# Kernel tuning notes

Hardware: AMD Instinct MI355X
Metric: run time of the kernel (lower is better)

The kernel has to match this reference:

```python
import jax, jax.numpy as jnp
import numpy as np

H = 768          # hidden size
NH = 12          # num heads
HD = H // NH     # head dim = 64
I = 3072         # intermediate size
EPS = 1e-6


def setup_inputs() -> dict:
    key = jax.random.key(0)
    ks = jax.random.split(key, 16)
    s = 1.0 / np.sqrt(H)
    si = 1.0 / np.sqrt(I)
    return {
        "hidden_states": jax.random.normal(ks[0], (16, 1024, H), jnp.float32),
        # attention projections (torch Linear: weight [out, in])
        "wq": jax.random.normal(ks[1], (H, H), jnp.float32) * s,
        "bq": jnp.zeros((H,), jnp.float32),
        "wk": jax.random.normal(ks[2], (H, H), jnp.float32) * s,
        "bk": jnp.zeros((H,), jnp.float32),
        "wv": jax.random.normal(ks[3], (H, H), jnp.float32) * s,
        "bv": jnp.zeros((H,), jnp.float32),
        "wo": jax.random.normal(ks[4], (H, H), jnp.float32) * s,
        "bo": jnp.zeros((H,), jnp.float32),
        # layer norms
        "ln1_g": jnp.ones((H,), jnp.float32),
        "ln1_b": jnp.zeros((H,), jnp.float32),
        "ln2_g": jnp.ones((H,), jnp.float32),
        "ln2_b": jnp.zeros((H,), jnp.float32),
        # MLP
        "w1": jax.random.normal(ks[5], (I, H), jnp.float32) * s,
        "b1": jnp.zeros((I,), jnp.float32),
        "w2": jax.random.normal(ks[6], (H, I), jnp.float32) * si,
        "b2": jnp.zeros((H,), jnp.float32),
    }


def _layer_norm(x, g, b):
    mu = jnp.mean(x, axis=-1, keepdims=True)
    var = jnp.var(x, axis=-1, keepdims=True)
    return (x - mu) * jax.lax.rsqrt(var + EPS) * g + b


def _linear(x, w, b):
    return jnp.einsum('bsi,oi->bso', x, w) + b


def reference(hidden_states, wq, bq, wk, bk, wv, bv, wo, bo,
              ln1_g, ln1_b, ln2_g, ln2_b, w1, b1, w2, b2):
    B, S, _ = hidden_states.shape
    scale = HD ** -0.5

    # attention block
    residual = hidden_states
    x = _layer_norm(hidden_states, ln1_g, ln1_b)
    q = _linear(x, wq, bq).reshape(B, S, NH, HD).transpose(0, 2, 1, 3)
    k = _linear(x, wk, bk).reshape(B, S, NH, HD).transpose(0, 2, 1, 3)
    v = _linear(x, wv, bv).reshape(B, S, NH, HD).transpose(0, 2, 1, 3)
    scores = jnp.einsum('bhqd,bhkd->bhqk', q, k) * scale   # [B,NH,S,S]
    attn = jax.nn.softmax(scores, axis=-1)
    o = jnp.einsum('bhqk,bhkd->bhqd', attn, v)
    o = o.transpose(0, 2, 1, 3).reshape(B, S, H)
    x = residual + _linear(o, wo, bo)

    # MLP block
    residual = x
    y = _layer_norm(x, ln2_g, ln2_b)
    y = jax.nn.gelu(_linear(y, w1, b1), approximate=True)  # tanh approx
    y = _linear(y, w2, b2)
    return residual + y
```

## Files before the change

### kernel.cpp

```cpp
#include <hip/hip_runtime.h>
#include <hip/hip_bf16.h>


#define H_ 768
#define I_ 3072
#define NTOK 16384
#define SEQ 1024
#define NH_ 12

typedef __attribute__((ext_vector_type(8))) __bf16 bf16x8;
typedef __attribute__((ext_vector_type(4))) __bf16 bf16x4;
typedef __attribute__((ext_vector_type(4))) float  f32x4;

__device__ __forceinline__ void gll16(const void* g, void* l) {
  __builtin_amdgcn_global_load_lds(
      (const __attribute__((address_space(1))) unsigned int*)g,
      (__attribute__((address_space(3))) unsigned int*)l, 16, 0, 0);
}

__global__ __launch_bounds__(256) void f2b(const float* __restrict__ s,
                                           __bf16* __restrict__ d, int n) {
  int i = (blockIdx.x * 256 + threadIdx.x) * 4;
  if (i >= n) return;
  f32x4 v = *(const f32x4*)&s[i];
  bf16x4 o;
  #pragma unroll
  for (int j = 0; j < 4; ++j) o[j] = (__bf16)v[j];
  *(bf16x4*)&d[i] = o;
}

__global__ __launch_bounds__(256) void ln_fwd(const float* __restrict__ x,
                                              const float* __restrict__ gg,
                                              const float* __restrict__ bb,
                                              __bf16* __restrict__ y) {
  const int row  = blockIdx.x * 4 + (threadIdx.x >> 6);
  const int lane = threadIdx.x & 63;
  const float* xr = x + (size_t)row * H_;
  f32x4 v[3];
  float s = 0.f, ss = 0.f;
  #pragma unroll
  for (int i = 0; i < 3; ++i) {
    v[i] = *(const f32x4*)&xr[lane * 4 + i * 256];
    #pragma unroll
    for (int j = 0; j < 4; ++j) { s += v[i][j]; ss += v[i][j] * v[i][j]; }
  }
  #pragma unroll
  for (int d = 1; d < 64; d <<= 1) { s += __shfl_xor(s, d); ss += __shfl_xor(ss, d); }
  const float mu   = s * (1.0f / 768.0f);
  const float var  = ss * (1.0f / 768.0f) - mu * mu;
  const float rstd = rsqrtf(var + 1e-6f);
  #pragma unroll
  for (int i = 0; i < 3; ++i) {
    const int c0 = lane * 4 + i * 256;
    f32x4 g4 = *(const f32x4*)&gg[c0];
    f32x4 b4 = *(const f32x4*)&bb[c0];
    bf16x4 o;
    #pragma unroll
    for (int j = 0; j < 4; ++j) o[j] = (__bf16)((v[i][j] - mu) * rstd * g4[j] + b4[j]);
    *(bf16x4*)&y[(size_t)row * H_ + c0] = o;
  }
}

template <int EPI>
__global__ __launch_bounds__(256) void gemm_bt(const __bf16* __restrict__ A,
                                               const __bf16* __restrict__ B,
                                               const float* __restrict__ bias,
                                               const float* __restrict__ res,
                                               void* __restrict__ Cv, int N, int K) {
  __shared__ __bf16 sA[128 * 64];
  __shared__ __bf16 sB[128 * 64];
  const int tid = threadIdx.x, lane = tid & 63, w = tid >> 6;
  const int lg = lane >> 4, lm = lane & 15;
  const int wr = w >> 1, wc = w & 1;
  const int m0 = blockIdx.y * 128, n0 = blockIdx.x * 128;
  const int rsub = lane >> 3;
  const int gcol = (lane & 7) ^ rsub;

  const __bf16* abase = A + (size_t)(m0 + w * 32 + rsub) * K + gcol * 8;
  const __bf16* bbase = B + (size_t)(n0 + w * 32 + rsub) * K + gcol * 8;

  f32x4 acc[4][4] = {};

  const int nkt = K >> 6;
  for (int kt = 0; kt < nkt; ++kt) {
    __syncthreads();
    #pragma unroll
    for (int j = 0; j < 4; ++j) {
      gll16(abase + (size_t)j * 8 * K + kt * 64, (char*)sA + (w * 4 + j) * 1024);
      gll16(bbase + (size_t)j * 8 * K + kt * 64, (char*)sB + (w * 4 + j) * 1024);
    }
    __syncthreads();

    bf16x8 af[4][2], bfr[4][2];
    #pragma unroll
    for (int f = 0; f < 4; ++f) {
      #pragma unroll
      for (int ks = 0; ks < 2; ++ks) {
        const int ra = wr * 64 + f * 16 + lm;
        const int pa = (lg + ks * 4) ^ (ra & 7);
        af[f][ks] = *(const bf16x8*)&sA[ra * 64 + pa * 8];
        const int rb = wc * 64 + f * 16 + lm;
        const int pb = (lg + ks * 4) ^ (rb & 7);
        bfr[f][ks] = *(const bf16x8*)&sB[rb * 64 + pb * 8];
      }
    }
    #pragma unroll
    for (int ks = 0; ks < 2; ++ks)
      #pragma unroll
      for (int mf = 0; mf < 4; ++mf)
        #pragma unroll
        for (int nf = 0; nf < 4; ++nf)
          acc[mf][nf] = __builtin_amdgcn_mfma_f32_16x16x32_bf16(
              af[mf][ks], bfr[nf][ks], acc[mf][nf], 0, 0, 0);
  }

  #pragma unroll
  for (int nf = 0; nf < 4; ++nf) {
    const int col = n0 + wc * 64 + nf * 16 + lm;
    const float bi = bias[col];
    #pragma unroll
    for (int mf = 0; mf < 4; ++mf) {
      #pragma unroll
      for (int q = 0; q < 4; ++q) {
        const size_t row = (size_t)(m0 + wr * 64 + mf * 16 + lg * 4 + q);
        float v = acc[mf][nf][q] + bi;
        if constexpr (EPI == 1) {
          const float u = 0.7978845608028654f * (v + 0.044715f * v * v * v);
          v = v / (1.0f + __expf(-2.0f * u));
        }
        if constexpr (EPI == 2) {
          v += res[row * N + col];
          ((float*)Cv)[row * N + col] = v;
        } else {
          ((__bf16*)Cv)[row * N + col] = (__bf16)v;
        }
      }
    }
  }
}

__global__ __launch_bounds__(256) void vtrans(const __bf16* __restrict__ qkv,
                                              __bf16* __restrict__ vt) {
  __shared__ __bf16 t[64][72];
  const int b = blockIdx.z, h = blockIdx.y, st = blockIdx.x;
  const int tid = threadIdx.x;
  const int r = tid >> 2, s2 = (tid & 3) * 2;
  const __bf16* src = qkv + (size_t)(b * SEQ + st * 64 + r) * 2304 + 1536 + h * 64;
  *(bf16x8*)&t[r][s2 * 8]     = *(const bf16x8*)&src[s2 * 8];
  *(bf16x8*)&t[r][s2 * 8 + 8] = *(const bf16x8*)&src[s2 * 8 + 8];
  __syncthreads();
  __bf16* dst = vt + (size_t)((b * NH_ + h) * 64 + r) * SEQ + st * 64;
  bf16x8 a, c;
  #pragma unroll
  for (int j = 0; j < 8; ++j) { a[j] = t[s2 * 8 + j][r]; c[j] = t[s2 * 8 + 8 + j][r]; }
  *(bf16x8*)&dst[s2 * 8]     = a;
  *(bf16x8*)&dst[s2 * 8 + 8] = c;
}

__global__ __launch_bounds__(256) void attn_fwd(const __bf16* __restrict__ qkv,
                                                const __bf16* __restrict__ vt,
                                                __bf16* __restrict__ o) {
  __shared__ __bf16 sK[64 * 64];
  __shared__ __bf16 sV[64 * 64];
  __shared__ __bf16 sP[4][32 * 64];
  const int b = blockIdx.z, h = blockIdx.y, qt = blockIdx.x;
  const int tid = threadIdx.x, lane = tid & 63, w = tid >> 6;
  const int lg = lane >> 4, lm = lane & 15;
  const size_t rowbase = (size_t)b * SEQ + qt * 128 + w * 32;

  bf16x8 qf[2][2];
  #pragma unroll
  for (int mf = 0; mf < 2; ++mf)
    #pragma unroll
    for (int ks = 0; ks < 2; ++ks) {
      const __bf16* src = qkv + (rowbase + mf * 16 + lm) * 2304 + h * 64 + lg * 8 + ks * 32;
      bf16x8 t = *(const bf16x8*)src;
      #pragma unroll
      for (int j = 0; j < 8; ++j) t[j] = (__bf16)((float)t[j] * 0.125f);
      qf[mf][ks] = t;
    }

  float mreg[2][4], lreg[2][4];
  f32x4 oacc[2][4] = {};
  #pragma unroll
  for (int mf = 0; mf < 2; ++mf)
    #pragma unroll
    for (int q = 0; q < 4; ++q) { mreg[mf][q] = -3.0e38f; lreg[mf][q] = 0.f; }

  const int rsub = lane >> 3;
  const int gcol = (lane & 7) ^ rsub;
  const __bf16* kbase = qkv + (size_t)b * SEQ * 2304 + 768 + h * 64 + gcol * 8;
  const __bf16* vbase = vt + (size_t)((b * NH_ + h) * 64) * SEQ + gcol * 8;

  for (int kt = 0; kt < 16; ++kt) {
    __syncthreads();
    #pragma unroll
    for (int i = 0; i < 2; ++i) {
      const int r = (w * 2 + i) * 8 + rsub;
      gll16(kbase + (size_t)(kt * 64 + r) * 2304, (char*)sK + (w * 2 + i) * 1024);
      gll16(vbase + (size_t)r * SEQ + kt * 64,    (char*)sV + (w * 2 + i) * 1024);
    }
    __syncthreads();

    f32x4 sc[2][4] = {};
    bf16x8 kf[4][2];
    #pragma unroll
    for (int nf = 0; nf < 4; ++nf)
      #pragma unroll
      for (int ks = 0; ks < 2; ++ks) {
        const int row = nf * 16 + lm;
        const int ph  = (lg + ks * 4) ^ (row & 7);
        kf[nf][ks] = *(const bf16x8*)&sK[row * 64 + ph * 8];
      }
    #pragma unroll
    for (int ks = 0; ks < 2; ++ks)
      #pragma unroll
      for (int mf = 0; mf < 2; ++mf)
        #pragma unroll
        for (int nf = 0; nf < 4; ++nf)
          sc[mf][nf] = __builtin_amdgcn_mfma_f32_16x16x32_bf16(
              qf[mf][ks], kf[nf][ks], sc[mf][nf], 0, 0, 0);

    #pragma unroll
    for (int mf = 0; mf < 2; ++mf) {
      #pragma unroll
      for (int q = 0; q < 4; ++q) {
        float tm = fmaxf(fmaxf(sc[mf][0][q], sc[mf][1][q]),
                         fmaxf(sc[mf][2][q], sc[mf][3][q]));
        tm = fmaxf(tm, __shfl_xor(tm, 1));
        tm = fmaxf(tm, __shfl_xor(tm, 2));
        tm = fmaxf(tm, __shfl_xor(tm, 4));
        tm = fmaxf(tm, __shfl_xor(tm, 8));
        const float mo = mreg[mf][q];
        const float mn = fmaxf(mo, tm);
        const float f  = __expf(mo - mn);
        mreg[mf][q] = mn;
        float rs = 0.f;
        #pragma unroll
        for (int nf = 0; nf < 4; ++nf) {
          const float p = __expf(sc[mf][nf][q] - mn);
          sc[mf][nf][q] = p;
          rs += p;
        }
        rs += __shfl_xor(rs, 1); rs += __shfl_xor(rs, 2);
        rs += __shfl_xor(rs, 4); rs += __shfl_xor(rs, 8);
        lreg[mf][q] = lreg[mf][q] * f + rs;
        #pragma unroll
        for (int nd = 0; nd < 4; ++nd) oacc[mf][nd][q] *= f;
      }
    }

    __bf16* pw = sP[w];
    #pragma unroll
    for (int mf = 0; mf < 2; ++mf)
      #pragma unroll
      for (int nf = 0; nf < 4; ++nf)
        #pragma unroll
        for (int q = 0; q < 4; ++q) {
          const int row = mf * 16 + lg * 4 + q;
          const int col = nf * 16 + lm;
          const int ph  = (col >> 3) ^ (row & 7);
          pw[row * 64 + ph * 8 + (col & 7)] = (__bf16)sc[mf][nf][q];
        }
    asm volatile("s_waitcnt lgkmcnt(0)" ::: "memory");

    bf16x8 pf[2][2], vf[4][2];
    #pragma unroll
    for (int mf = 0; mf < 2; ++mf)
      #pragma unroll
      for (int ks = 0; ks < 2; ++ks) {
        const int row = mf * 16 + lm;
        const int ph  = (lg + ks * 4) ^ (row & 7);
        pf[mf][ks] = *(const bf16x8*)&pw[row * 64 + ph * 8];
      }
    #pragma unroll
    for (int nf = 0; nf < 4; ++nf)
      #pragma unroll
      for (int ks = 0; ks < 2; ++ks) {
        const int d  = nf * 16 + lm;
        const int ph = (lg + ks * 4) ^ (d & 7);
        vf[nf][ks] = *(const bf16x8*)&sV[d * 64 + ph * 8];
      }
    #pragma unroll
    for (int ks = 0; ks < 2; ++ks)
      #pragma unroll
      for (int mf = 0; mf < 2; ++mf)
        #pragma unroll
        for (int nf = 0; nf < 4; ++nf)
          oacc[mf][nf] = __builtin_amdgcn_mfma_f32_16x16x32_bf16(
              pf[mf][ks], vf[nf][ks], oacc[mf][nf], 0, 0, 0);
  }

  #pragma unroll
  for (int mf = 0; mf < 2; ++mf) {
    #pragma unroll
    for (int q = 0; q < 4; ++q) {
      const float inv = 1.0f / lreg[mf][q];
      const size_t row = rowbase + mf * 16 + lg * 4 + q;
      #pragma unroll
      for (int nf = 0; nf < 4; ++nf) {
        const int col = h * 64 + nf * 16 + lm;
        o[row * H_ + col] = (__bf16)(oacc[mf][nf][q] * inv);
      }
    }
  }
}

extern "C" void kernel_launch(void* const* d_in, const int* in_sizes, int n_in,
                              void* d_out, int out_size, void* d_ws, size_t ws_size,
                              hipStream_t stream) {
  const float* hs   = (const float*)d_in[0];
  const float* wq   = (const float*)d_in[1];
  const float* bq   = (const float*)d_in[2];
  const float* wk   = (const float*)d_in[3];
  const float* bk   = (const float*)d_in[4];
  const float* wv   = (const float*)d_in[5];
  const float* bv   = (const float*)d_in[6];
  const float* wo   = (const float*)d_in[7];
  const float* bo   = (const float*)d_in[8];
  const float* ln1g = (const float*)d_in[9];
  const float* ln1b = (const float*)d_in[10];
  const float* ln2g = (const float*)d_in[11];
  const float* ln2b = (const float*)d_in[12];
  const float* w1   = (const float*)d_in[13];
  const float* b1   = (const float*)d_in[14];
  const float* w2   = (const float*)d_in[15];
  const float* b2   = (const float*)d_in[16];

  char* ws = (char*)d_ws;
  __bf16* wqkv = (__bf16*)(ws);
  __bf16* wo_b = (__bf16*)(ws + 3538944);
  __bf16* w1_b = (__bf16*)(ws + 4718592);
  __bf16* w2_b = (__bf16*)(ws + 9437184);
  float*  bqkv = (float*) (ws + 14155776);
  __bf16* xn   = (__bf16*)(ws + 14164992);
  __bf16* ob   = xn;
  __bf16* qkv  = (__bf16*)(ws + 39330816);
  __bf16* vt   = (__bf16*)(ws + 114828288);
  __bf16* gb   = (__bf16*)(ws + 39330816);
  float*  x2   = (float*)d_out;

  hipMemcpyAsync(bqkv,        bq, 768 * sizeof(float), hipMemcpyDeviceToDevice, stream);
  hipMemcpyAsync(bqkv + 768,  bk, 768 * sizeof(float), hipMemcpyDeviceToDevice, stream);
  hipMemcpyAsync(bqkv + 1536, bv, 768 * sizeof(float), hipMemcpyDeviceToDevice, stream);

  f2b<<<576, 256, 0, stream>>>(wq, wqkv,            589824);
  f2b<<<576, 256, 0, stream>>>(wk, wqkv + 589824,   589824);
  f2b<<<576, 256, 0, stream>>>(wv, wqkv + 1179648,  589824);
  f2b<<<576, 256, 0, stream>>>(wo, wo_b,            589824);
  f2b<<<2304, 256, 0, stream>>>(w1, w1_b,           2359296);
  f2b<<<2304, 256, 0, stream>>>(w2, w2_b,           2359296);

  ln_fwd<<<4096, 256, 0, stream>>>(hs, ln1g, ln1b, xn);
  gemm_bt<0><<<dim3(18, 128), 256, 0, stream>>>(xn, wqkv, bqkv, nullptr, qkv, 2304, 768);
  vtrans<<<dim3(16, 12, 16), 256, 0, stream>>>(qkv, vt);
  attn_fwd<<<dim3(8, 12, 16), 256, 0, stream>>>(qkv, vt, ob);
  gemm_bt<2><<<dim3(6, 128), 256, 0, stream>>>(ob, wo_b, bo, hs, (void*)x2, 768, 768);
  ln_fwd<<<4096, 256, 0, stream>>>(x2, ln2g, ln2b, xn);
  gemm_bt<1><<<dim3(24, 128), 256, 0, stream>>>(xn, w1_b, b1, nullptr, gb, 3072, 768);
  gemm_bt<2><<<dim3(6, 128), 256, 0, stream>>>(gb, w2_b, b2, x2, (void*)d_out, 768, 3072);
}
```

Measured before the change: 700.3 us.

## Compute transposed S=K·Q^T in attention to keep P in registers, remap blocks per XCD

The attention kernel now computes scores as K·Q^T so each lane holds P values laid out as the B operand of a 16x16x16 bf16 MFMA. P then feeds the PV product straight from registers, which removes the per-warp LDS round-trip for P and its waitcnt. Row reductions become cross-lane shuffles over 16/32 plus in-register max/sum, and the output is written as 4-wide vectors. The grid is also flattened so that consecutive work items (the same batch-head) land on the same XCD for L2 reuse of K/V. The cost is the older 16x16x16 MFMA with half the K depth, so twice as many MFMA issues for PV, and smaller V fragment reads from LDS.

```diff
diff --git a/kernel.cpp b/kernel.cpp
--- a/kernel.cpp
+++ b/kernel.cpp
@@ -11,11 +11,22 @@
 typedef __attribute__((ext_vector_type(8))) __bf16 bf16x8;
 typedef __attribute__((ext_vector_type(4))) __bf16 bf16x4;
 typedef __attribute__((ext_vector_type(4))) float  f32x4;
+typedef __attribute__((ext_vector_type(4))) short  s16x4;
 
 __device__ __forceinline__ void gll16(const void* g, void* l) {
   __builtin_amdgcn_global_load_lds(
       (const __attribute__((address_space(1))) unsigned int*)g,
       (__attribute__((address_space(3))) unsigned int*)l, 16, 0, 0);
+}
+
+__device__ __forceinline__ f32x4 mfma16x16x16bf16(s16x4 a, s16x4 b, f32x4 c) {
+#if __has_builtin(__builtin_amdgcn_mfma_f32_16x16x16bf16_1k)
+  return __builtin_amdgcn_mfma_f32_16x16x16bf16_1k(a, b, c, 0, 0, 0);
+#else
+  asm volatile("v_mfma_f32_16x16x16_bf16 %0, %1, %2, %0"
+               : "+v"(c) : "v"(a), "v"(b));
+  return c;
+#endif
 }
 
 __global__ __launch_bounds__(256) void f2b(const float* __restrict__ s,
@@ -162,30 +173,31 @@
                                                 __bf16* __restrict__ o) {
   __shared__ __bf16 sK[64 * 64];
   __shared__ __bf16 sV[64 * 64];
-  __shared__ __bf16 sP[4][32 * 64];
-  const int b = blockIdx.z, h = blockIdx.y, qt = blockIdx.x;
+  const int lin = blockIdx.x;
+  const int xcd = lin & 7, slot = lin >> 3;
+  const int workid = xcd * 192 + slot;
+  const int qt = workid & 7;
+  const int bh = workid >> 3;
+  const int b = bh / NH_, h = bh % NH_;
   const int tid = threadIdx.x, lane = tid & 63, w = tid >> 6;
   const int lg = lane >> 4, lm = lane & 15;
   const size_t rowbase = (size_t)b * SEQ + qt * 128 + w * 32;
 
   bf16x8 qf[2][2];
   #pragma unroll
-  for (int mf = 0; mf < 2; ++mf)
+  for (int qb = 0; qb < 2; ++qb)
     #pragma unroll
     for (int ks = 0; ks < 2; ++ks) {
-      const __bf16* src = qkv + (rowbase + mf * 16 + lm) * 2304 + h * 64 + lg * 8 + ks * 32;
+      const __bf16* src = qkv + (rowbase + qb * 16 + lm) * 2304 + h * 64 + ks * 32 + lg * 8;
       bf16x8 t = *(const bf16x8*)src;
       #pragma unroll
       for (int j = 0; j < 8; ++j) t[j] = (__bf16)((float)t[j] * 0.125f);
-      qf[mf][ks] = t;
-    }
-
-  float mreg[2][4], lreg[2][4];
-  f32x4 oacc[2][4] = {};
-  #pragma unroll
-  for (int mf = 0; mf < 2; ++mf)
-    #pragma unroll
-    for (int q = 0; q < 4; ++q) { mreg[mf][q] = -3.0e38f; lreg[mf][q] = 0.f; }
+      qf[qb][ks] = t;
+    }
+
+  float mreg[2] = {-3.0e38f, -3.0e38f};
+  float lreg[2] = {0.f, 0.f};
+  f32x4 oacc[4][2] = {};
 
   const int rsub = lane >> 3;
   const int gcol = (lane & 7) ^ rsub;
@@ -202,106 +214,93 @@
     }
     __syncthreads();
 
-    f32x4 sc[2][4] = {};
     bf16x8 kf[4][2];
     #pragma unroll
-    for (int nf = 0; nf < 4; ++nf)
+    for (int kb = 0; kb < 4; ++kb)
       #pragma unroll
       for (int ks = 0; ks < 2; ++ks) {
-        const int row = nf * 16 + lm;
+        const int row = kb * 16 + lm;
         const int ph  = (lg + ks * 4) ^ (row & 7);
-        kf[nf][ks] = *(const bf16x8*)&sK[row * 64 + ph * 8];
-      }
+        kf[kb][ks] = *(const bf16x8*)&sK[row * 64 + ph * 8];
+      }
+    f32x4 sc[4][2] = {};
     #pragma unroll
     for (int ks = 0; ks < 2; ++ks)
       #pragma unroll
-      for (int mf = 0; mf < 2; ++mf)
-        #pragma unroll
-        for (int nf = 0; nf < 4; ++nf)
-          sc[mf][nf] = __builtin_amdgcn_mfma_f32_16x16x32_bf16(
-              qf[mf][ks], kf[nf][ks], sc[mf][nf], 0, 0, 0);
-
-    #pragma unroll
-    for (int mf = 0; mf < 2; ++mf) {
-      #pragma unroll
-      for (int q = 0; q < 4; ++q) {
-        float tm = fmaxf(fmaxf(sc[mf][0][q], sc[mf][1][q]),
-                         fmaxf(sc[mf][2][q], sc[mf][3][q]));
-        tm = fmaxf(tm, __shfl_xor(tm, 1));
-        tm = fmaxf(tm, __shfl_xor(tm, 2));
-        tm = fmaxf(tm, __shfl_xor(tm, 4));
-        tm = fmaxf(tm, __shfl_xor(tm, 8));
-        const float mo = mreg[mf][q];
-        const float mn = fmaxf(mo, tm);
-        const float f  = __expf(mo - mn);
-        mreg[mf][q] = mn;
-        float rs = 0.f;
-        #pragma unroll
-        for (int nf = 0; nf < 4; ++nf) {
-          const float p = __expf(sc[mf][nf][q] - mn);
-          sc[mf][nf][q] = p;
+      for (int kb = 0; kb < 4; ++kb)
+        #pragma unroll
+        for (int qb = 0; qb < 2; ++qb)
+          sc[kb][qb] = __builtin_amdgcn_mfma_f32_16x16x32_bf16(
+              kf[kb][ks], qf[qb][ks], sc[kb][qb], 0, 0, 0);
+
+    #pragma unroll
+    for (int qb = 0; qb < 2; ++qb) {
+      float t0 = fmaxf(fmaxf(sc[0][qb][0], sc[0][qb][1]), fmaxf(sc[0][qb][2], sc[0][qb][3]));
+      float t1 = fmaxf(fmaxf(sc[1][qb][0], sc[1][qb][1]), fmaxf(sc[1][qb][2], sc[1][qb][3]));
+      float t2 = fmaxf(fmaxf(sc[2][qb][0], sc[2][qb][1]), fmaxf(sc[2][qb][2], sc[2][qb][3]));
+      float t3 = fmaxf(fmaxf(sc[3][qb][0], sc[3][qb][1]), fmaxf(sc[3][qb][2], sc[3][qb][3]));
+      float tm = fmaxf(fmaxf(t0, t1), fmaxf(t2, t3));
+      tm = fmaxf(tm, __shfl_xor(tm, 16));
+      tm = fmaxf(tm, __shfl_xor(tm, 32));
+      const float mo = mreg[qb];
+      const float mn = fmaxf(mo, tm);
+      const float f  = __expf(mo - mn);
+      mreg[qb] = mn;
+      float rs = 0.f;
+      #pragma unroll
+      for (int kb = 0; kb < 4; ++kb)
+        #pragma unroll
+        for (int r = 0; r < 4; ++r) {
+          const float p = __expf(sc[kb][qb][r] - mn);
+          sc[kb][qb][r] = p;
           rs += p;
         }
-        rs += __shfl_xor(rs, 1); rs += __shfl_xor(rs, 2);
-        rs += __shfl_xor(rs, 4); rs += __shfl_xor(rs, 8);
-        lreg[mf][q] = lreg[mf][q] * f + rs;
-        #pragma unroll
-        for (int nd = 0; nd < 4; ++nd) oacc[mf][nd][q] *= f;
-      }
-    }
-
-    __bf16* pw = sP[w];
-    #pragma unroll
-    for (int mf = 0; mf < 2; ++mf)
-      #pragma unroll
-      for (int nf = 0; nf < 4; ++nf)
-        #pragma unroll
-        for (int q = 0; q < 4; ++q) {
-          const int row = mf * 16 + lg * 4 + q;
-          const int col = nf * 16 + lm;
-          const int ph  = (col >> 3) ^ (row & 7);
-          pw[row * 64 + ph * 8 + (col & 7)] = (__bf16)sc[mf][nf][q];
-        }
-    asm volatile("s_waitcnt lgkmcnt(0)" ::: "memory");
-
-    bf16x8 pf[2][2], vf[4][2];
-    #pragma unroll
-    for (int mf = 0; mf < 2; ++mf)
-      #pragma unroll
-      for (int ks = 0; ks < 2; ++ks) {
-        const int row = mf * 16 + lm;
-        const int ph  = (lg + ks * 4) ^ (row & 7);
-        pf[mf][ks] = *(const bf16x8*)&pw[row * 64 + ph * 8];
-      }
-    #pragma unroll
-    for (int nf = 0; nf < 4; ++nf)
-      #pragma unroll
-      for (int ks = 0; ks < 2; ++ks) {
-        const int d  = nf * 16 + lm;
-        const int ph = (lg + ks * 4) ^ (d & 7);
-        vf[nf][ks] = *(const bf16x8*)&sV[d * 64 + ph * 8];
-      }
-    #pragma unroll
-    for (int ks = 0; ks < 2; ++ks)
-      #pragma unroll
-      for (int mf = 0; mf < 2; ++mf)
-        #pragma unroll
-        for (int nf = 0; nf < 4; ++nf)
-          oacc[mf][nf] = __builtin_amdgcn_mfma_f32_16x16x32_bf16(
-              pf[mf][ks], vf[nf][ks], oacc[mf][nf], 0, 0, 0);
-  }
-
-  #pragma unroll
-  for (int mf = 0; mf < 2; ++mf) {
-    #pragma unroll
-    for (int q = 0; q < 4; ++q) {
-      const float inv = 1.0f / lreg[mf][q];
-      const size_t row = rowbase + mf * 16 + lg * 4 + q;
-      #pragma unroll
-      for (int nf = 0; nf < 4; ++nf) {
-        const int col = h * 64 + nf * 16 + lm;
-        o[row * H_ + col] = (__bf16)(oacc[mf][nf][q] * inv);
-      }
+      rs += __shfl_xor(rs, 16);
+      rs += __shfl_xor(rs, 32);
+      lreg[qb] = lreg[qb] * f + rs;
+      #pragma unroll
+      for (int db = 0; db < 4; ++db)
+        #pragma unroll
+        for (int r = 0; r < 4; ++r) oacc[db][qb][r] *= f;
+    }
+
+    s16x4 pb[4][2];
+    #pragma unroll
+    for (int kb = 0; kb < 4; ++kb)
+      #pragma unroll
+      for (int qb = 0; qb < 2; ++qb) {
+        union { bf16x4 h; s16x4 s; } u;
+        #pragma unroll
+        for (int r = 0; r < 4; ++r) u.h[r] = (__bf16)sc[kb][qb][r];
+        pb[kb][qb] = u.s;
+      }
+
+    #pragma unroll
+    for (int kb = 0; kb < 4; ++kb) {
+      const int kv0 = kb * 16 + lg * 4;
+      const int sl  = kv0 >> 3;
+      const int off = kv0 & 7;
+      #pragma unroll
+      for (int db = 0; db < 4; ++db) {
+        const int d = db * 16 + lm;
+        const s16x4 va = *(const s16x4*)&sV[d * 64 + (sl ^ (d & 7)) * 8 + off];
+        #pragma unroll
+        for (int qb = 0; qb < 2; ++qb)
+          oacc[db][qb] = mfma16x16x16bf16(va, pb[kb][qb], oacc[db][qb]);
+      }
+    }
+  }
+
+  #pragma unroll
+  for (int qb = 0; qb < 2; ++qb) {
+    const float inv = 1.0f / lreg[qb];
+    const size_t row = rowbase + qb * 16 + lm;
+    #pragma unroll
+    for (int db = 0; db < 4; ++db) {
+      bf16x4 ov;
+      #pragma unroll
+      for (int r = 0; r < 4; ++r) ov[r] = (__bf16)(oacc[db][qb][r] * inv);
+      *(bf16x4*)&o[row * H_ + h * 64 + db * 16 + lg * 4] = ov;
     }
   }
 }
@@ -354,7 +353,7 @@
   ln_fwd<<<4096, 256, 0, stream>>>(hs, ln1g, ln1b, xn);
   gemm_bt<0><<<dim3(18, 128), 256, 0, stream>>>(xn, wqkv, bqkv, nullptr, qkv, 2304, 768);
   vtrans<<<dim3(16, 12, 16), 256, 0, stream>>>(qkv, vt);
-  attn_fwd<<<dim3(8, 12, 16), 256, 0, stream>>>(qkv, vt, ob);
+  attn_fwd<<<1536, 256, 0, stream>>>(qkv, vt, ob);
   gemm_bt<2><<<dim3(6, 128), 256, 0, stream>>>(ob, wo_b, bo, hs, (void*)x2, 768, 768);
   ln_fwd<<<4096, 256, 0, stream>>>(x2, ln2g, ln2b, xn);
   gemm_bt<1><<<dim3(24, 128), 256, 0, stream>>>(xn, w1_b, b1, nullptr, gb, 3072, 768);
```

Result: faster. 667.4 us (-4.7%).
